# Kernel tuning notes

Hardware: AMD Instinct MI355X
Metric: run time of the kernel (lower is better)

Reference implementation:

```python
import jax, jax.numpy as jnp
import numpy as np

N_NODES = 50000
N_EDGES = 500000
IN_FEAT = 128
OUT_FEAT = 128
N_REL = 16


def setup_inputs() -> dict:
    key = jax.random.key(0)
    k1, k2, k3, k4 = jax.random.split(key, 4)
    entity_embeddings = jax.random.normal(k1, (N_NODES, IN_FEAT), dtype=jnp.float32)
    # xavier_uniform over (in, out) fan per relation slice
    limit = (6.0 / (IN_FEAT + OUT_FEAT)) ** 0.5
    weight = jax.random.uniform(k2, (N_REL, IN_FEAT, OUT_FEAT), dtype=jnp.float32,
                                minval=-limit, maxval=limit)
    edge_index = jax.random.randint(k3, (2, N_EDGES), 0, N_NODES, dtype=jnp.int64)
    edge_type = jax.random.randint(k4, (N_EDGES,), 0, N_REL, dtype=jnp.int64)
    return {"entity_embeddings": entity_embeddings, "weight": weight,
            "edge_index": edge_index, "edge_type": edge_type}


def reference(entity_embeddings, weight, edge_index, edge_type):
    # RGCN message passing: for each edge e with relation r:
    #   msg_e = x[src_e] @ W[r];  out[tgt_e] += msg_e;  out = relu(out)
    # Vectorized: transform every node by every relation once (R*N*in*out flops),
    # then gather the (relation, src) slice per edge and scatter-add to tgt.
    # This avoids gathering a per-edge (E, in, out) weight tensor.
    num_entities = entity_embeddings.shape[0]
    src = edge_index[0]
    tgt = edge_index[1]
    transformed = jnp.einsum('ni,rio->rno', entity_embeddings, weight)  # (R, N, O)
    msg = transformed[edge_type, src]                                   # (E, O)
    messages = jax.ops.segment_sum(msg, tgt, num_segments=num_entities)  # (N, O)
    # Dropout is identity in eval mode; reference omits it (deterministic baseline).
    return jax.nn.relu(messages)
```

## Files before the change

kernel.cpp:

```cpp
#include <hip/hip_runtime.h>
#include <hip/hip_bf16.h>

typedef __attribute__((ext_vector_type(8))) __bf16 bf16x8;
typedef __attribute__((ext_vector_type(4))) __bf16 bf16x4;
typedef __attribute__((ext_vector_type(4))) float f32x4;

#define IN_FEAT 128
#define OUT_FEAT 128
#define N_REL 16
#define TILE_M 64
#define CHUNK_T 4

__global__ __launch_bounds__(256) void prep_kernel(
        const float* __restrict__ w, __bf16* __restrict__ wt,
        const float* __restrict__ x, __bf16* __restrict__ xb, int nX, int cvtb,
        const int* __restrict__ etype, const int* __restrict__ etgt, int n,
        int* __restrict__ cnt_rel, int* __restrict__ cnt_tgt) {
    __shared__ __bf16 tile[32 * 136];
    __shared__ int h[N_REL];
    int t = threadIdx.x;
    if (blockIdx.x < 64) {
        int r = blockIdx.x >> 2;
        int n0 = (blockIdx.x & 3) * 32;
        const float* W = w + (size_t)r * IN_FEAT * OUT_FEAT;
        __bf16* T = wt + (size_t)r * IN_FEAT * OUT_FEAT;
        #pragma unroll
        for (int it = 0; it < 16; ++it) {
            int idx = t + it * 256;
            int k = idx >> 5, dn = idx & 31;
            tile[dn * 136 + k] = (__bf16)W[k * OUT_FEAT + n0 + dn];
        }
        __syncthreads();
        #pragma unroll
        for (int it = 0; it < 2; ++it) {
            int idx = t + it * 256;
            int nn = idx >> 4, c = idx & 15;
            bf16x8 v = *(const bf16x8*)(&tile[nn * 136 + c * 8]);
            *(bf16x8*)(T + (size_t)(n0 + nn) * IN_FEAT + c * 8) = v;
        }
    } else if (blockIdx.x < 64 + cvtb) {
        int i = ((blockIdx.x - 64) * 256 + t) * 8;
        if (i < nX) {
            const float4* xr = (const float4*)(x + i);
            float4 f0 = xr[0], f1 = xr[1];
            bf16x8 o = { (__bf16)f0.x, (__bf16)f0.y, (__bf16)f0.z, (__bf16)f0.w,
                         (__bf16)f1.x, (__bf16)f1.y, (__bf16)f1.z, (__bf16)f1.w };
            *(bf16x8*)(xb + i) = o;
        }
    } else {
        if (t < N_REL) h[t] = 0;
        __syncthreads();
        int stride = (gridDim.x - 64 - cvtb) * blockDim.x;
        for (int i = (blockIdx.x - 64 - cvtb) * blockDim.x + t; i < n; i += stride) {
            atomicAdd(&h[etype[i]], 1);
            atomicAdd(&cnt_tgt[etgt[i]], 1);
        }
        __syncthreads();
        if (t < N_REL) atomicAdd(&cnt_rel[t], h[t]);
    }
}

__global__ void hist_kernel(const int* __restrict__ etype, int n, int* __restrict__ cnt_rel) {
    __shared__ int h[N_REL];
    if (threadIdx.x < N_REL) h[threadIdx.x] = 0;
    __syncthreads();
    for (int i = blockIdx.x * blockDim.x + threadIdx.x; i < n; i += gridDim.x * blockDim.x)
        atomicAdd(&h[etype[i]], 1);
    __syncthreads();
    if (threadIdx.x < N_REL) atomicAdd(&cnt_rel[threadIdx.x], h[threadIdx.x]);
}
__global__ void prefix_kernel(const int* __restrict__ cnt, int* __restrict__ meta) {
    if (threadIdx.x == 0) {
        int off = 0, toff = 0;
        for (int r = 0; r < N_REL; ++r) {
            meta[r] = off; meta[32 + r] = toff; meta[64 + r] = off;
            off += cnt[r];
            toff += (cnt[r] + TILE_M - 1) / TILE_M;
        }
        meta[16] = off; meta[48] = toff;
    }
}

__global__ void scanA_kernel(const int* __restrict__ cnt, int n, int* __restrict__ partial) {
    __shared__ int s[256];
    int i = blockIdx.x * 256 + threadIdx.x;
    s[threadIdx.x] = (i < n) ? cnt[i] : 0;
    __syncthreads();
    for (int off = 128; off > 0; off >>= 1) {
        if (threadIdx.x < off) s[threadIdx.x] += s[threadIdx.x + off];
        __syncthreads();
    }
    if (threadIdx.x == 0) partial[blockIdx.x] = s[0];
}
__global__ void scanC2_kernel(const int* __restrict__ cnt, int n,
                              const int* __restrict__ partial,
                              const int* __restrict__ cnt_rel, int* __restrict__ meta,
                              int* __restrict__ base, int* __restrict__ cursor) {
    __shared__ int s[256];
    __shared__ int sbase;
    int t = threadIdx.x;
    int pb = 0;
    for (int i = t; i < (int)blockIdx.x; i += 256) pb += partial[i];
    s[t] = pb;
    __syncthreads();
    for (int off = 128; off > 0; off >>= 1) {
        if (t < off) s[t] += s[t + off];
        __syncthreads();
    }
    if (t == 0) sbase = s[0];
    __syncthreads();
    int blockbase = sbase;
    __syncthreads();
    int i = blockIdx.x * 256 + t;
    int v = (i < n) ? cnt[i] : 0;
    s[t] = v;
    __syncthreads();
    for (int off = 1; off < 256; off <<= 1) {
        int x = (t >= off) ? s[t - off] : 0;
        __syncthreads();
        s[t] += x;
        __syncthreads();
    }
    int b = blockbase + s[t] - v;
    if (i < n) { base[i] = b; cursor[i] = b; }
    if (blockIdx.x == 0 && t == 0) {
        int off = 0, toff = 0;
        for (int r = 0; r < N_REL; ++r) {
            meta[r] = off; meta[32 + r] = toff; meta[64 + r] = off;
            off += cnt_rel[r];
            toff += (cnt_rel[r] + TILE_M - 1) / TILE_M;
        }
        meta[16] = off; meta[48] = toff;
    }
}

#define SCATTER_EPT 2
#define SCATTER_CHUNK (256 * SCATTER_EPT)
__global__ __launch_bounds__(256) void scatter_slot_kernel(
        const int* __restrict__ esrc, const int* __restrict__ etgt,
        const int* __restrict__ etype, int n,
        int* __restrict__ cursor_rel, int* __restrict__ cursor_tgt,
        int* __restrict__ bsrc, int* __restrict__ bslot) {
    __shared__ int lcnt[N_REL];
    __shared__ int lbase[N_REL];
    int t = threadIdx.x;
    if (t < N_REL) lcnt[t] = 0;
    __syncthreads();
    int base = blockIdx.x * SCATTER_CHUNK;
    int rj[SCATTER_EPT], offj[SCATTER_EPT];
    #pragma unroll
    for (int j = 0; j < SCATTER_EPT; ++j) {
        int i = base + j * 256 + t;
        if (i < n) {
            int r = etype[i];
            rj[j] = r;
            offj[j] = atomicAdd(&lcnt[r], 1);
        } else rj[j] = -1;
    }
    __syncthreads();
    if (t < N_REL) lbase[t] = atomicAdd(&cursor_rel[t], lcnt[t]);
    __syncthreads();
    #pragma unroll
    for (int j = 0; j < SCATTER_EPT; ++j) {
        if (rj[j] >= 0) {
            int i = base + j * 256 + t;
            int p = lbase[rj[j]] + offj[j];
            bsrc[p] = esrc[i];
            bslot[p] = atomicAdd(&cursor_tgt[etgt[i]], 1);
        }
    }
}

__global__ __launch_bounds__(256) void scatter_kernel(
        const int* __restrict__ esrc, const int* __restrict__ etgt,
        const int* __restrict__ etype, int n,
        int* __restrict__ cursor,
        int* __restrict__ bsrc, int* __restrict__ btgt) {
    __shared__ int lcnt[N_REL];
    __shared__ int lbase[N_REL];
    int t = threadIdx.x;
    if (t < N_REL) lcnt[t] = 0;
    __syncthreads();
    int base = blockIdx.x * SCATTER_CHUNK;
    int rj[SCATTER_EPT], offj[SCATTER_EPT];
    #pragma unroll
    for (int j = 0; j < SCATTER_EPT; ++j) {
        int i = base + j * 256 + t;
        if (i < n) {
            int r = etype[i];
            rj[j] = r;
            offj[j] = atomicAdd(&lcnt[r], 1);
        } else rj[j] = -1;
    }
    __syncthreads();
    if (t < N_REL) lbase[t] = atomicAdd(&cursor[t], lcnt[t]);
    __syncthreads();
    #pragma unroll
    for (int j = 0; j < SCATTER_EPT; ++j) {
        if (rj[j] >= 0) {
            int i = base + j * 256 + t;
            int p = lbase[rj[j]] + offj[j];
            bsrc[p] = esrc[i];
            btgt[p] = etgt[i];
        }
    }
}

__global__ __launch_bounds__(256) void gemm_msg7_kernel(
    const __bf16* __restrict__ Xb,
    const __bf16* __restrict__ Wt,
    const int* __restrict__ bsrc, const int* __restrict__ bslot,
    const int* __restrict__ meta,
    __bf16* __restrict__ msg) {
    __shared__ __align__(16) __bf16 Bs[OUT_FEAT * 128];
    __shared__ __align__(16) __bf16 As[TILE_M * 128];
    __shared__ int s_slot[TILE_M];

    const int* rel_off = meta;
    const int* tile_pre = meta + 32;
    int T = tile_pre[16];
    int t0 = blockIdx.x * CHUNK_T;
    if (t0 >= T) return;
    int t1 = min(T, t0 + CHUNK_T);

    int tid = threadIdx.x;
    int wave = tid >> 6, lane = tid & 63;
    int q = lane >> 4, ln = lane & 15;
    uint4* BsV = (uint4*)Bs;
    uint4* AsV = (uint4*)As;
    const bf16x8* AsF = (const bf16x8*)As;
    const bf16x8* BsF = (const bf16x8*)Bs;

    int cur_rel = -1;
    for (int tt = t0; tt < t1; ++tt) {
        int rel = (cur_rel < 0) ? 0 : cur_rel;
        while (tt >= tile_pre[rel + 1]) ++rel;
        int tile = tt - tile_pre[rel];
        int row_start = rel_off[rel] + tile * TILE_M;
        int m_valid = min(TILE_M, rel_off[rel + 1] - row_start);

        __syncthreads();
        if (rel != cur_rel) {
            cur_rel = rel;
            const __bf16* wsrc = Wt + (size_t)rel * IN_FEAT * OUT_FEAT;
            #pragma unroll
            for (int i = 0; i < 8; ++i) {
                int cid = tid + i * 256;
                int row = cid >> 4, c = cid & 15;
                int feat = (row & 15) * 8 + (row >> 4);
                uint4 v = *(const uint4*)(wsrc + (size_t)feat * IN_FEAT + c * 8);
                BsV[row * 16 + (c ^ (row & 15))] = v;
            }
        }
        #pragma unroll
        for (int i = 0; i < 4; ++i) {
            int cid = tid + i * 256;
            int r = cid >> 4, c = cid & 15;
            int srcn = (r < m_valid) ? bsrc[row_start + r] : 0;
            uint4 v = *(const uint4*)(Xb + (size_t)srcn * IN_FEAT + c * 8);
            AsV[r * 16 + (c ^ (r & 15))] = v;
        }
        if (tid < TILE_M) s_slot[tid] = (tid < m_valid) ? bslot[row_start + tid] : -1;
        __syncthreads();

        f32x4 acc[8];
        f32x4 z = { 0.f, 0.f, 0.f, 0.f };
        #pragma unroll
        for (int nf = 0; nf < 8; ++nf) acc[nf] = z;

        int myrow = wave * 16 + ln;
        #pragma unroll
        for (int kk = 0; kk < 4; ++kk) {
            bf16x8 a = AsF[myrow * 16 + ((kk * 4 + q) ^ ln)];
            #pragma unroll
            for (int nf = 0; nf < 8; ++nf) {
                bf16x8 b = BsF[(nf * 16 + ln) * 16 + ((kk * 4 + q) ^ ln)];
                acc[nf] = __builtin_amdgcn_mfma_f32_16x16x32_bf16(a, b, acc[nf], 0, 0, 0);
            }
        }

        #pragma unroll
        for (int reg = 0; reg < 4; ++reg) {
            int row = wave * 16 + q * 4 + reg;
            int slot = s_slot[row];
            if (slot >= 0) {
                bf16x8 o = { (__bf16)acc[0][reg], (__bf16)acc[1][reg],
                             (__bf16)acc[2][reg], (__bf16)acc[3][reg],
                             (__bf16)acc[4][reg], (__bf16)acc[5][reg],
                             (__bf16)acc[6][reg], (__bf16)acc[7][reg] };
                *(bf16x8*)(msg + (size_t)slot * OUT_FEAT + ln * 8) = o;
            }
        }
    }
}

__global__ __launch_bounds__(256) void segsum4_kernel(
        const __bf16* __restrict__ msg, const int* __restrict__ base,
        int nnodes, int ntot, float* __restrict__ out) {
    int n = blockIdx.x * 4 + (threadIdx.x >> 6);
    if (n >= nnodes) return;
    int l = threadIdx.x & 63;
    int g = l >> 4, ln = l & 15;
    int s0 = base[n];
    int s1 = (n == nnodes - 1) ? ntot : base[n + 1];
    float a[8] = { 0.f, 0.f, 0.f, 0.f, 0.f, 0.f, 0.f, 0.f };
    for (int s = s0 + g; s < s1; s += 8) {
        bf16x8 m0 = *(const bf16x8*)(msg + (size_t)s * OUT_FEAT + ln * 8);
        if (s + 4 < s1) {
            bf16x8 m1 = *(const bf16x8*)(msg + (size_t)(s + 4) * OUT_FEAT + ln * 8);
            #pragma unroll
            for (int j = 0; j < 8; ++j) a[j] += (float)m0[j] + (float)m1[j];
        } else {
            #pragma unroll
            for (int j = 0; j < 8; ++j) a[j] += (float)m0[j];
        }
    }
    #pragma unroll
    for (int j = 0; j < 8; ++j) {
        a[j] += __shfl_xor(a[j], 16, 64);
        a[j] += __shfl_xor(a[j], 32, 64);
    }
    if (g == 0) {
        float4 o0 = { fmaxf(a[0], 0.f), fmaxf(a[1], 0.f), fmaxf(a[2], 0.f), fmaxf(a[3], 0.f) };
        float4 o1 = { fmaxf(a[4], 0.f), fmaxf(a[5], 0.f), fmaxf(a[6], 0.f), fmaxf(a[7], 0.f) };
        float* dst = out + (size_t)n * OUT_FEAT + ln * 8;
        *(float4*)dst = o0;
        *(float4*)(dst + 4) = o1;
    }
}

__global__ void cvtX_kernel(const float* __restrict__ x, __bf16* __restrict__ xb, int n) {
    int i = (blockIdx.x * blockDim.x + threadIdx.x) * 4;
    if (i < n) {
        float4 v = *(const float4*)(x + i);
        bf16x4 o = { (__bf16)v.x, (__bf16)v.y, (__bf16)v.z, (__bf16)v.w };
        *(bf16x4*)(xb + i) = o;
    }
}
#define LDA 136
__global__ __launch_bounds__(256) void gemm_scatter_kernel(
    const __bf16* __restrict__ Xb, const __bf16* __restrict__ Wt,
    const int* __restrict__ bsrc, const int* __restrict__ btgt,
    const int* __restrict__ meta, float* __restrict__ out) {
    __shared__ __align__(16) __bf16 As2[TILE_M * LDA];
    __shared__ __align__(16) __bf16 Bs2[OUT_FEAT * LDA];
    __shared__ int s_tgt[TILE_M];
    int bid = blockIdx.x;
    const int* rel_off = meta;
    const int* tile_pre = meta + 32;
    if (bid >= tile_pre[16]) return;
    int rel = 0;
    while (bid >= tile_pre[rel + 1]) rel++;
    int tile = bid - tile_pre[rel];
    int row_start = rel_off[rel] + tile * TILE_M;
    int m_valid = min(TILE_M, rel_off[rel + 1] - row_start);
    int t = threadIdx.x;
    {
        const __bf16* src = Wt + rel * IN_FEAT * OUT_FEAT;
        #pragma unroll
        for (int i = 0; i < 8; ++i) {
            int cid = t + i * 256;
            int n = cid >> 4, c = cid & 15;
            uint4 v = *(const uint4*)(src + n * IN_FEAT + c * 8);
            *(uint4*)(&Bs2[n * LDA + c * 8]) = v;
        }
    }
    {
        #pragma unroll
        for (int i = 0; i < 4; ++i) {
            int cid = t + i * 256;
            int r = cid >> 4, c = cid & 15;
            int srcn = (r < m_valid) ? bsrc[row_start + r] : 0;
            uint4 v = *(const uint4*)(Xb + srcn * IN_FEAT + c * 8);
            *(uint4*)(&As2[r * LDA + c * 8]) = v;
        }
        if (t < TILE_M) s_tgt[t] = (t < m_valid) ? btgt[row_start + t] : -1;
    }
    __syncthreads();
    int wave = t >> 6, lane = t & 63;
    int q = lane >> 4, ln = lane & 15;
    f32x4 acc[8];
    f32x4 z = { 0.f, 0.f, 0.f, 0.f };
    #pragma unroll
    for (int nf = 0; nf < 8; ++nf) acc[nf] = z;
    #pragma unroll
    for (int kk = 0; kk < 4; ++kk) {
        bf16x8 a = *(const bf16x8*)(&As2[(wave * 16 + ln) * LDA + kk * 32 + q * 8]);
        #pragma unroll
        for (int nf = 0; nf < 8; ++nf) {
            bf16x8 b = *(const bf16x8*)(&Bs2[(nf * 16 + ln) * LDA + kk * 32 + q * 8]);
            acc[nf] = __builtin_amdgcn_mfma_f32_16x16x32_bf16(a, b, acc[nf], 0, 0, 0);
        }
    }
    #pragma unroll
    for (int reg = 0; reg < 4; ++reg) {
        int r = wave * 16 + q * 4 + reg;
        int tgt = s_tgt[r];
        if (tgt >= 0) {
            float* orow = out + (size_t)tgt * OUT_FEAT + ln;
            #pragma unroll
            for (int nf = 0; nf < 8; ++nf)
                unsafeAtomicAdd(orow + nf * 16, acc[nf][reg]);
        }
    }
}
__global__ void relu_kernel(float* __restrict__ out, int n) {
    int i = (blockIdx.x * blockDim.x + threadIdx.x) * 4;
    if (i < n) {
        float4 v = *(float4*)(out + i);
        v.x = fmaxf(v.x, 0.f); v.y = fmaxf(v.y, 0.f);
        v.z = fmaxf(v.z, 0.f); v.w = fmaxf(v.w, 0.f);
        *(float4*)(out + i) = v;
    }
}

extern "C" void kernel_launch(void* const* d_in, const int* in_sizes, int n_in,
                              void* d_out, int out_size, void* d_ws, size_t ws_size,
                              hipStream_t stream) {
    const float* x = (const float*)d_in[0];
    const float* w = (const float*)d_in[1];
    const int* eidx = (const int*)d_in[2];
    const int* etype = (const int*)d_in[3];
    const int E = in_sizes[3];
    const int nX = in_sizes[0];
    const int N = out_size / OUT_FEAT;
    const int* esrc = eidx;
    const int* etgt = eidx + E;
    float* out = (float*)d_out;

    char* ws = (char*)d_ws;
    size_t off = 0;
    auto alloc = [&](size_t sz) { size_t o = off; off = (off + sz + 255) & ~(size_t)255; return o; };
    size_t off_Xb   = alloc((size_t)nX * 2);
    size_t off_Wt   = alloc((size_t)N_REL * IN_FEAT * OUT_FEAT * 2);
    size_t off_cnt  = alloc(64);
    size_t off_meta = alloc(512);
    size_t off_bsrc = alloc((size_t)E * 4);
    size_t off_bsl  = alloc((size_t)E * 4);
    size_t off_ctgt = alloc((size_t)(N + 16) * 4);
    size_t off_cur  = alloc((size_t)N * 4);
    size_t off_base = alloc((size_t)N * 4);
    size_t off_part = alloc(1024);
    size_t off_msg  = alloc((size_t)E * OUT_FEAT * 2);
    bool big = (ws_size >= off);

    __bf16* Xb = (__bf16*)(ws + off_Xb);
    __bf16* Wt = (__bf16*)(ws + off_Wt);
    int* meta  = (int*)(ws + off_meta);
    int* bsrc  = (int*)(ws + off_bsrc);
    int* bsl   = (int*)(ws + off_bsl);

    int scatter_blocks = (E + SCATTER_CHUNK - 1) / SCATTER_CHUNK;
    int max_tiles = (E + TILE_M - 1) / TILE_M + N_REL;

    if (big) {
        int* cnt_tgt = (int*)(ws + off_ctgt);
        int* cnt_rel = cnt_tgt + N;
        int* cursor  = (int*)(ws + off_cur);
        int* base    = (int*)(ws + off_base);
        int* partial = (int*)(ws + off_part);
        __bf16* msg  = (__bf16*)(ws + off_msg);
        int nchunks = (N + 255) / 256;
        int cvtb = (nX / 8 + 255) / 256;

        hipMemsetAsync(cnt_tgt, 0, (size_t)(N + 16) * 4, stream);
        prep_kernel<<<64 + cvtb + 1024, 256, 0, stream>>>(
            w, Wt, x, Xb, nX, cvtb, etype, etgt, E, cnt_rel, cnt_tgt);
        scanA_kernel<<<nchunks, 256, 0, stream>>>(cnt_tgt, N, partial);
        scanC2_kernel<<<nchunks, 256, 0, stream>>>(cnt_tgt, N, partial, cnt_rel, meta, base, cursor);
        scatter_slot_kernel<<<scatter_blocks, 256, 0, stream>>>(
            esrc, etgt, etype, E, meta + 64, cursor, bsrc, bsl);
        int gemm_blocks = (max_tiles + CHUNK_T - 1) / CHUNK_T;
        gemm_msg7_kernel<<<gemm_blocks, 256, 0, stream>>>(Xb, Wt, bsrc, bsl, meta, msg);
        segsum4_kernel<<<(N + 3) / 4, 256, 0, stream>>>(msg, base, N, E, out);
    } else {
        int* cnt = (int*)(ws + off_cnt);
        hipMemsetAsync(cnt, 0, 64, stream);
        hipMemsetAsync(out, 0, (size_t)out_size * 4, stream);
        cvtX_kernel<<<(nX / 4 + 255) / 256, 256, 0, stream>>>(x, Xb, nX);
        prep_kernel<<<64, 256, 0, stream>>>(w, Wt, x, Xb, 0, 0, etype, etgt, E, cnt, nullptr);
        hist_kernel<<<1024, 256, 0, stream>>>(etype, E, cnt);
        prefix_kernel<<<1, 64, 0, stream>>>(cnt, meta);
        scatter_kernel<<<scatter_blocks, 256, 0, stream>>>(
            esrc, etgt, etype, E, meta + 64, bsrc, bsl);
        gemm_scatter_kernel<<<max_tiles, 256, 0, stream>>>(Xb, Wt, bsrc, bsl, meta, out);
        relu_kernel<<<(out_size / 4 + 255) / 256, 256, 0, stream>>>(out, out_size);
    }
}
```

Baseline: 223.5 us.

## Fuse whole RGCN pipeline into one cooperative persistent kernel with grid syncs

Replaces the memset plus six separate kernel launches with a single cooperative kernel of 512 blocks. The stages (zeroing, weight transpose and X conversion, histogram, scan, scatter, GEMM, segment sum with ReLU) are separated by grid.sync() calls. The aim is to remove per-launch overhead and inter-kernel gaps. In exchange, each stage now runs on a fixed grid, so the GEMM and segsum stages use far fewer blocks than before, and the grid-wide barriers add their own cost. If the cooperative launch fails, the old multi-kernel path is used instead.

New measurement: 621.5 us. +178.1%, slower.

```diff
diff --git a/kernel.cpp b/kernel.cpp
--- a/kernel.cpp
+++ b/kernel.cpp
@@ -1,5 +1,8 @@
 #include <hip/hip_runtime.h>
 #include <hip/hip_bf16.h>
+#include <hip/hip_cooperative_groups.h>
+
+namespace cg = cooperative_groups;
 
 typedef __attribute__((ext_vector_type(8))) __bf16 bf16x8;
 typedef __attribute__((ext_vector_type(4))) __bf16 bf16x4;
@@ -9,7 +12,268 @@
 #define OUT_FEAT 128
 #define N_REL 16
 #define TILE_M 64
-#define CHUNK_T 4
+#define FUSED_GRID 512
+#define SCATTER_EPT 2
+#define SCATTER_CHUNK (256 * SCATTER_EPT)
+
+__global__ __launch_bounds__(256, 2) void fused_kernel(
+    const float* __restrict__ x, const float* __restrict__ w,
+    const int* __restrict__ esrc, const int* __restrict__ etgt,
+    const int* __restrict__ etype, int E, int N, int nX,
+    __bf16* __restrict__ Xb, __bf16* __restrict__ Wt,
+    int* __restrict__ cnt_tgt,
+    int* __restrict__ meta, int* __restrict__ bsrc, int* __restrict__ bslot,
+    int* __restrict__ base, int* __restrict__ cursor, int* __restrict__ partial,
+    __bf16* __restrict__ msg, float* __restrict__ out) {
+    cg::grid_group grid = cg::this_grid();
+    __shared__ __align__(16) char smem[49664];
+    int bid = blockIdx.x, t = threadIdx.x;
+    int* cnt_rel = cnt_tgt + N;
+
+    for (int i = bid * 256 + t; i < N + 16; i += FUSED_GRID * 256) cnt_tgt[i] = 0;
+    grid.sync();
+
+    if (bid < 64) {
+        __bf16* tile = (__bf16*)smem;
+        int r = bid >> 2, n0 = (bid & 3) * 32;
+        const float* W = w + (size_t)r * IN_FEAT * OUT_FEAT;
+        __bf16* Tw = Wt + (size_t)r * IN_FEAT * OUT_FEAT;
+        #pragma unroll
+        for (int it = 0; it < 16; ++it) {
+            int idx = t + it * 256;
+            int k = idx >> 5, dn = idx & 31;
+            tile[dn * 136 + k] = (__bf16)W[k * OUT_FEAT + n0 + dn];
+        }
+        __syncthreads();
+        #pragma unroll
+        for (int it = 0; it < 2; ++it) {
+            int idx = t + it * 256;
+            int nn = idx >> 4, c = idx & 15;
+            bf16x8 v = *(const bf16x8*)(&tile[nn * 136 + c * 8]);
+            *(bf16x8*)(Tw + (size_t)(n0 + nn) * IN_FEAT + c * 8) = v;
+        }
+    } else {
+        int U = nX >> 3;
+        for (int u = (bid - 64) * 256 + t; u < U; u += (FUSED_GRID - 64) * 256) {
+            const float4* xr = (const float4*)(x + (size_t)u * 8);
+            float4 f0 = xr[0], f1 = xr[1];
+            bf16x8 o = { (__bf16)f0.x, (__bf16)f0.y, (__bf16)f0.z, (__bf16)f0.w,
+                         (__bf16)f1.x, (__bf16)f1.y, (__bf16)f1.z, (__bf16)f1.w };
+            *(bf16x8*)(Xb + (size_t)u * 8) = o;
+        }
+    }
+    {
+        int* h = (int*)(smem + 9216);
+        __syncthreads();
+        if (t < N_REL) h[t] = 0;
+        __syncthreads();
+        for (int i = bid * 256 + t; i < E; i += FUSED_GRID * 256) {
+            atomicAdd(&h[etype[i]], 1);
+            atomicAdd(&cnt_tgt[etgt[i]], 1);
+        }
+        __syncthreads();
+        if (t < N_REL) atomicAdd(&cnt_rel[t], h[t]);
+    }
+    grid.sync();
+
+    int nchunks = (N + 255) >> 8;
+    if (bid < nchunks) {
+        int* s = (int*)smem;
+        int i = bid * 256 + t;
+        s[t] = (i < N) ? cnt_tgt[i] : 0;
+        __syncthreads();
+        for (int off = 128; off > 0; off >>= 1) {
+            if (t < off) s[t] += s[t + off];
+            __syncthreads();
+        }
+        if (t == 0) partial[bid] = s[0];
+    }
+    grid.sync();
+    if (bid == 0) {
+        int* s = (int*)smem;
+        int v = (t < nchunks) ? partial[t] : 0;
+        s[t] = v;
+        __syncthreads();
+        for (int off = 1; off < 256; off <<= 1) {
+            int xz = (t >= off) ? s[t - off] : 0;
+            __syncthreads();
+            s[t] += xz;
+            __syncthreads();
+        }
+        if (t < nchunks) partial[t] = s[t] - v;
+        if (t == 0) {
+            int off = 0, toff = 0;
+            for (int r = 0; r < N_REL; ++r) {
+                meta[r] = off; meta[32 + r] = toff; meta[64 + r] = off;
+                off += cnt_rel[r];
+                toff += (cnt_rel[r] + TILE_M - 1) / TILE_M;
+            }
+            meta[16] = off; meta[48] = toff;
+        }
+    }
+    grid.sync();
+    if (bid < nchunks) {
+        int* s = (int*)smem;
+        int i = bid * 256 + t;
+        int v = (i < N) ? cnt_tgt[i] : 0;
+        s[t] = v;
+        __syncthreads();
+        for (int off = 1; off < 256; off <<= 1) {
+            int xz = (t >= off) ? s[t - off] : 0;
+            __syncthreads();
+            s[t] += xz;
+            __syncthreads();
+        }
+        int b = partial[bid] + s[t] - v;
+        if (i < N) { base[i] = b; cursor[i] = b; }
+    }
+    grid.sync();
+    {
+        int* lcnt = (int*)smem;
+        int* lbase = (int*)(smem + 64);
+        int* cursor_rel = meta + 64;
+        int nsc = (E + SCATTER_CHUNK - 1) / SCATTER_CHUNK;
+        for (int c = bid; c < nsc; c += FUSED_GRID) {
+            __syncthreads();
+            if (t < N_REL) lcnt[t] = 0;
+            __syncthreads();
+            int cb = c * SCATTER_CHUNK;
+            int rj[SCATTER_EPT], offj[SCATTER_EPT];
+            #pragma unroll
+            for (int j = 0; j < SCATTER_EPT; ++j) {
+                int i = cb + j * 256 + t;
+                if (i < E) {
+                    int r = etype[i];
+                    rj[j] = r;
+                    offj[j] = atomicAdd(&lcnt[r], 1);
+                } else rj[j] = -1;
+            }
+            __syncthreads();
+            if (t < N_REL) lbase[t] = atomicAdd(&cursor_rel[t], lcnt[t]);
+            __syncthreads();
+            #pragma unroll
+            for (int j = 0; j < SCATTER_EPT; ++j) {
+                if (rj[j] >= 0) {
+                    int i = cb + j * 256 + t;
+                    int p = lbase[rj[j]] + offj[j];
+                    bsrc[p] = esrc[i];
+                    bslot[p] = atomicAdd(&cursor[etgt[i]], 1);
+                }
+            }
+        }
+    }
+    grid.sync();
+    {
+        const int* rel_off = meta;
+        const int* tile_pre = meta + 32;
+        int Tt = tile_pre[16];
+        int chunk = (Tt + FUSED_GRID - 1) / FUSED_GRID;
+        int t0 = bid * chunk, t1 = min(Tt, t0 + chunk);
+        __bf16* Bs = (__bf16*)smem;
+        __bf16* As = (__bf16*)(smem + 32768);
+        int* s_slot = (int*)(smem + 49152);
+        uint4* BsV = (uint4*)Bs;
+        uint4* AsV = (uint4*)As;
+        const bf16x8* AsF = (const bf16x8*)As;
+        const bf16x8* BsF = (const bf16x8*)Bs;
+        int wave = t >> 6, lane = t & 63;
+        int q = lane >> 4, ln = lane & 15;
+        int cur_rel = -1;
+        for (int tt = t0; tt < t1; ++tt) {
+            int rel = (cur_rel < 0) ? 0 : cur_rel;
+            while (tt >= tile_pre[rel + 1]) ++rel;
+            int row_start = rel_off[rel] + (tt - tile_pre[rel]) * TILE_M;
+            int m_valid = min(TILE_M, rel_off[rel + 1] - row_start);
+            __syncthreads();
+            if (rel != cur_rel) {
+                cur_rel = rel;
+                const __bf16* wsrc = Wt + (size_t)rel * IN_FEAT * OUT_FEAT;
+                #pragma unroll
+                for (int i = 0; i < 8; ++i) {
+                    int cid = t + i * 256;
+                    int row = cid >> 4, c = cid & 15;
+                    int feat = (row & 15) * 8 + (row >> 4);
+                    uint4 v = *(const uint4*)(wsrc + (size_t)feat * IN_FEAT + c * 8);
+                    BsV[row * 16 + (c ^ (row & 15))] = v;
+                }
+            }
+            #pragma unroll
+            for (int i = 0; i < 4; ++i) {
+                int cid = t + i * 256;
+                int r = cid >> 4, c = cid & 15;
+                int srcn = (r < m_valid) ? bsrc[row_start + r] : 0;
+                uint4 v = *(const uint4*)(Xb + (size_t)srcn * IN_FEAT + c * 8);
+                AsV[r * 16 + (c ^ (r & 15))] = v;
+            }
+            if (t < TILE_M) s_slot[t] = (t < m_valid) ? bslot[row_start + t] : -1;
+            __syncthreads();
+
+            f32x4 acc[8];
+            f32x4 z = { 0.f, 0.f, 0.f, 0.f };
+            #pragma unroll
+            for (int nf = 0; nf < 8; ++nf) acc[nf] = z;
+            int myrow = wave * 16 + ln;
+            #pragma unroll
+            for (int kk = 0; kk < 4; ++kk) {
+                bf16x8 a = AsF[myrow * 16 + ((kk * 4 + q) ^ ln)];
+                #pragma unroll
+                for (int nf = 0; nf < 8; ++nf) {
+                    bf16x8 b = BsF[(nf * 16 + ln) * 16 + ((kk * 4 + q) ^ ln)];
+                    acc[nf] = __builtin_amdgcn_mfma_f32_16x16x32_bf16(a, b, acc[nf], 0, 0, 0);
+                }
+            }
+            #pragma unroll
+            for (int reg = 0; reg < 4; ++reg) {
+                int row = wave * 16 + q * 4 + reg;
+                int slot = s_slot[row];
+                if (slot >= 0) {
+                    bf16x8 o = { (__bf16)acc[0][reg], (__bf16)acc[1][reg],
+                                 (__bf16)acc[2][reg], (__bf16)acc[3][reg],
+                                 (__bf16)acc[4][reg], (__bf16)acc[5][reg],
+                                 (__bf16)acc[6][reg], (__bf16)acc[7][reg] };
+                    *(bf16x8*)(msg + (size_t)slot * OUT_FEAT + ln * 8) = o;
+                }
+            }
+        }
+    }
+    grid.sync();
+    {
+        int ngrp = (N + 3) >> 2;
+        int wv = t >> 6, l = t & 63;
+        int g = l >> 4, ln = l & 15;
+        for (int grp = bid; grp < ngrp; grp += FUSED_GRID) {
+            int n = grp * 4 + wv;
+            if (n < N) {
+                int s0 = base[n];
+                int s1 = (n == N - 1) ? E : base[n + 1];
+                float a[8] = { 0.f, 0.f, 0.f, 0.f, 0.f, 0.f, 0.f, 0.f };
+                for (int s = s0 + g; s < s1; s += 8) {
+                    bf16x8 m0 = *(const bf16x8*)(msg + (size_t)s * OUT_FEAT + ln * 8);
+                    if (s + 4 < s1) {
+                        bf16x8 m1 = *(const bf16x8*)(msg + (size_t)(s + 4) * OUT_FEAT + ln * 8);
+                        #pragma unroll
+                        for (int j = 0; j < 8; ++j) a[j] += (float)m0[j] + (float)m1[j];
+                    } else {
+                        #pragma unroll
+                        for (int j = 0; j < 8; ++j) a[j] += (float)m0[j];
+                    }
+                }
+                #pragma unroll
+                for (int j = 0; j < 8; ++j) {
+                    a[j] += __shfl_xor(a[j], 16, 64);
+                    a[j] += __shfl_xor(a[j], 32, 64);
+                }
+                if (g == 0) {
+                    float4 o0 = { fmaxf(a[0], 0.f), fmaxf(a[1], 0.f), fmaxf(a[2], 0.f), fmaxf(a[3], 0.f) };
+                    float4 o1 = { fmaxf(a[4], 0.f), fmaxf(a[5], 0.f), fmaxf(a[6], 0.f), fmaxf(a[7], 0.f) };
+                    float* dst = out + (size_t)n * OUT_FEAT + ln * 8;
+                    *(float4*)dst = o0;
+                    *(float4*)(dst + 4) = o1;
+                }
+            }
+        }
+    }
+}
 
 __global__ __launch_bounds__(256) void prep_kernel(
         const float* __restrict__ w, __bf16* __restrict__ wt,
@@ -53,7 +317,7 @@
         int stride = (gridDim.x - 64 - cvtb) * blockDim.x;
         for (int i = (blockIdx.x - 64 - cvtb) * blockDim.x + t; i < n; i += stride) {
             atomicAdd(&h[etype[i]], 1);
-            atomicAdd(&cnt_tgt[etgt[i]], 1);
+            if (cnt_tgt) atomicAdd(&cnt_tgt[etgt[i]], 1);
         }
         __syncthreads();
         if (t < N_REL) atomicAdd(&cnt_rel[t], h[t]);
@@ -134,8 +398,6 @@
     }
 }
 
-#define SCATTER_EPT 2
-#define SCATTER_CHUNK (256 * SCATTER_EPT)
 __global__ __launch_bounds__(256) void scatter_slot_kernel(
         const int* __restrict__ esrc, const int* __restrict__ etgt,
         const int* __restrict__ etype, int n,
@@ -206,23 +468,20 @@
     }
 }
 
+#define CHUNK_T 4
 __global__ __launch_bounds__(256) void gemm_msg7_kernel(
-    const __bf16* __restrict__ Xb,
-    const __bf16* __restrict__ Wt,
+    const __bf16* __restrict__ Xb, const __bf16* __restrict__ Wt,
     const int* __restrict__ bsrc, const int* __restrict__ bslot,
-    const int* __restrict__ meta,
-    __bf16* __restrict__ msg) {
+    const int* __restrict__ meta, __bf16* __restrict__ msg) {
     __shared__ __align__(16) __bf16 Bs[OUT_FEAT * 128];
     __shared__ __align__(16) __bf16 As[TILE_M * 128];
     __shared__ int s_slot[TILE_M];
-
     const int* rel_off = meta;
     const int* tile_pre = meta + 32;
     int T = tile_pre[16];
     int t0 = blockIdx.x * CHUNK_T;
     if (t0 >= T) return;
     int t1 = min(T, t0 + CHUNK_T);
-
     int tid = threadIdx.x;
     int wave = tid >> 6, lane = tid & 63;
     int q = lane >> 4, ln = lane & 15;
@@ -230,15 +489,12 @@
     uint4* AsV = (uint4*)As;
     const bf16x8* AsF = (const bf16x8*)As;
     const bf16x8* BsF = (const bf16x8*)Bs;
-
     int cur_rel = -1;
     for (int tt = t0; tt < t1; ++tt) {
         int rel = (cur_rel < 0) ? 0 : cur_rel;
         while (tt >= tile_pre[rel + 1]) ++rel;
-        int tile = tt - tile_pre[rel];
-        int row_start = rel_off[rel] + tile * TILE_M;
+        int row_start = rel_off[rel] + (tt - tile_pre[rel]) * TILE_M;
         int m_valid = min(TILE_M, rel_off[rel + 1] - row_start);
-
         __syncthreads();
         if (rel != cur_rel) {
             cur_rel = rel;
@@ -262,12 +518,10 @@
         }
         if (tid < TILE_M) s_slot[tid] = (tid < m_valid) ? bslot[row_start + tid] : -1;
         __syncthreads();
-
         f32x4 acc[8];
         f32x4 z = { 0.f, 0.f, 0.f, 0.f };
         #pragma unroll
         for (int nf = 0; nf < 8; ++nf) acc[nf] = z;
-
         int myrow = wave * 16 + ln;
         #pragma unroll
         for (int kk = 0; kk < 4; ++kk) {
@@ -278,7 +532,6 @@
                 acc[nf] = __builtin_amdgcn_mfma_f32_16x16x32_bf16(a, b, acc[nf], 0, 0, 0);
             }
         }
-
         #pragma unroll
         for (int reg = 0; reg < 4; ++reg) {
             int row = wave * 16 + q * 4 + reg;
@@ -460,19 +713,30 @@
         int* base    = (int*)(ws + off_base);
         int* partial = (int*)(ws + off_part);
         __bf16* msg  = (__bf16*)(ws + off_msg);
-        int nchunks = (N + 255) / 256;
-        int cvtb = (nX / 8 + 255) / 256;
-
-        hipMemsetAsync(cnt_tgt, 0, (size_t)(N + 16) * 4, stream);
-        prep_kernel<<<64 + cvtb + 1024, 256, 0, stream>>>(
-            w, Wt, x, Xb, nX, cvtb, etype, etgt, E, cnt_rel, cnt_tgt);
-        scanA_kernel<<<nchunks, 256, 0, stream>>>(cnt_tgt, N, partial);
-        scanC2_kernel<<<nchunks, 256, 0, stream>>>(cnt_tgt, N, partial, cnt_rel, meta, base, cursor);
-        scatter_slot_kernel<<<scatter_blocks, 256, 0, stream>>>(
-            esrc, etgt, etype, E, meta + 64, cursor, bsrc, bsl);
-        int gemm_blocks = (max_tiles + CHUNK_T - 1) / CHUNK_T;
-        gemm_msg7_kernel<<<gemm_blocks, 256, 0, stream>>>(Xb, Wt, bsrc, bsl, meta, msg);
-        segsum4_kernel<<<(N + 3) / 4, 256, 0, stream>>>(msg, base, N, E, out);
+
+        int Ev = E, Nv = N, nXv = nX;
+        void* args[] = { (void*)&x, (void*)&w, (void*)&esrc, (void*)&etgt, (void*)&etype,
+                         (void*)&Ev, (void*)&Nv, (void*)&nXv,
+                         (void*)&Xb, (void*)&Wt, (void*)&cnt_tgt, (void*)&meta,
+                         (void*)&bsrc, (void*)&bsl, (void*)&base, (void*)&cursor,
+                         (void*)&partial, (void*)&msg, (void*)&out };
+        hipError_t cerr = hipLaunchCooperativeKernel(
+            (const void*)fused_kernel, dim3(FUSED_GRID), dim3(256), args, 0, stream);
+        if (cerr != hipSuccess) {
+            (void)hipGetLastError();
+            int nchunks = (N + 255) / 256;
+            int cvtb = (nX / 8 + 255) / 256;
+            hipMemsetAsync(cnt_tgt, 0, (size_t)(N + 16) * 4, stream);
+            prep_kernel<<<64 + cvtb + 1024, 256, 0, stream>>>(
+                w, Wt, x, Xb, nX, cvtb, etype, etgt, E, cnt_rel, cnt_tgt);
+            scanA_kernel<<<nchunks, 256, 0, stream>>>(cnt_tgt, N, partial);
+            scanC2_kernel<<<nchunks, 256, 0, stream>>>(cnt_tgt, N, partial, cnt_rel, meta, base, cursor);
+            scatter_slot_kernel<<<scatter_blocks, 256, 0, stream>>>(
+                esrc, etgt, etype, E, meta + 64, cursor, bsrc, bsl);
+            int gemm_blocks = (max_tiles + CHUNK_T - 1) / CHUNK_T;
+            gemm_msg7_kernel<<<gemm_blocks, 256, 0, stream>>>(Xb, Wt, bsrc, bsl, meta, msg);
+            segsum4_kernel<<<(N + 3) / 4, 256, 0, stream>>>(msg, base, N, E, out);
+        }
     } else {
         int* cnt = (int*)(ws + off_cnt);
         hipMemsetAsync(cnt, 0, 64, stream);
```

## Load gathered A fragments directly into registers, drop A tile from LDS

Applied to the files above, without the earlier changes.

The gather GEMM kernel no longer stages the gathered source rows in shared memory. Each lane loads its MFMA A fragments straight from global memory and keeps the slot indices in registers. This removes two per-tile barriers and the A/slot shared buffers, shrinking LDS use so more blocks can be resident, and the launch bounds now request 4 blocks per SM. Each block also handles 8 tiles instead of 4, so the relation weights are reloaded less often, at the cost of fewer blocks and uncoalesced per-lane row loads. A null check on the target-count histogram is added as well.

After: 208.6 us. -6.6%, faster.

```diff
diff --git a/kernel.cpp b/kernel.cpp
--- a/kernel.cpp
+++ b/kernel.cpp
@@ -9,7 +9,7 @@
 #define OUT_FEAT 128
 #define N_REL 16
 #define TILE_M 64
-#define CHUNK_T 4
+#define CHUNK_T 8
 
 __global__ __launch_bounds__(256) void prep_kernel(
         const float* __restrict__ w, __bf16* __restrict__ wt,
@@ -53,7 +53,7 @@
         int stride = (gridDim.x - 64 - cvtb) * blockDim.x;
         for (int i = (blockIdx.x - 64 - cvtb) * blockDim.x + t; i < n; i += stride) {
             atomicAdd(&h[etype[i]], 1);
-            atomicAdd(&cnt_tgt[etgt[i]], 1);
+            if (cnt_tgt) atomicAdd(&cnt_tgt[etgt[i]], 1);
         }
         __syncthreads();
         if (t < N_REL) atomicAdd(&cnt_rel[t], h[t]);
@@ -206,16 +206,13 @@
     }
 }
 
-__global__ __launch_bounds__(256) void gemm_msg7_kernel(
+__global__ __launch_bounds__(256, 4) void gemm_msg8_kernel(
     const __bf16* __restrict__ Xb,
     const __bf16* __restrict__ Wt,
     const int* __restrict__ bsrc, const int* __restrict__ bslot,
     const int* __restrict__ meta,
     __bf16* __restrict__ msg) {
     __shared__ __align__(16) __bf16 Bs[OUT_FEAT * 128];
-    __shared__ __align__(16) __bf16 As[TILE_M * 128];
-    __shared__ int s_slot[TILE_M];
-
     const int* rel_off = meta;
     const int* tile_pre = meta + 32;
     int T = tile_pre[16];
@@ -227,20 +224,18 @@
     int wave = tid >> 6, lane = tid & 63;
     int q = lane >> 4, ln = lane & 15;
     uint4* BsV = (uint4*)Bs;
-    uint4* AsV = (uint4*)As;
-    const bf16x8* AsF = (const bf16x8*)As;
     const bf16x8* BsF = (const bf16x8*)Bs;
+    int myrow = wave * 16 + ln;
 
     int cur_rel = -1;
     for (int tt = t0; tt < t1; ++tt) {
         int rel = (cur_rel < 0) ? 0 : cur_rel;
         while (tt >= tile_pre[rel + 1]) ++rel;
-        int tile = tt - tile_pre[rel];
-        int row_start = rel_off[rel] + tile * TILE_M;
+        int row_start = rel_off[rel] + (tt - tile_pre[rel]) * TILE_M;
         int m_valid = min(TILE_M, rel_off[rel + 1] - row_start);
 
-        __syncthreads();
         if (rel != cur_rel) {
+            if (cur_rel >= 0) __syncthreads();
             cur_rel = rel;
             const __bf16* wsrc = Wt + (size_t)rel * IN_FEAT * OUT_FEAT;
             #pragma unroll
@@ -251,44 +246,45 @@
                 uint4 v = *(const uint4*)(wsrc + (size_t)feat * IN_FEAT + c * 8);
                 BsV[row * 16 + (c ^ (row & 15))] = v;
             }
-        }
-        #pragma unroll
-        for (int i = 0; i < 4; ++i) {
-            int cid = tid + i * 256;
-            int r = cid >> 4, c = cid & 15;
-            int srcn = (r < m_valid) ? bsrc[row_start + r] : 0;
-            uint4 v = *(const uint4*)(Xb + (size_t)srcn * IN_FEAT + c * 8);
-            AsV[r * 16 + (c ^ (r & 15))] = v;
-        }
-        if (tid < TILE_M) s_slot[tid] = (tid < m_valid) ? bslot[row_start + tid] : -1;
-        __syncthreads();
+            __syncthreads();
+        }
+
+        int src = bsrc[row_start + min(myrow, m_valid - 1)];
+        const __bf16* xrow = Xb + (size_t)src * IN_FEAT;
+        bf16x8 afr[4];
+        #pragma unroll
+        for (int kk = 0; kk < 4; ++kk)
+            afr[kk] = *(const bf16x8*)(xrow + (kk * 4 + q) * 8);
+
+        int slot[4];
+        #pragma unroll
+        for (int reg = 0; reg < 4; ++reg) {
+            int r = wave * 16 + q * 4 + reg;
+            slot[reg] = (r < m_valid) ? bslot[row_start + r] : -1;
+        }
 
         f32x4 acc[8];
         f32x4 z = { 0.f, 0.f, 0.f, 0.f };
         #pragma unroll
         for (int nf = 0; nf < 8; ++nf) acc[nf] = z;
 
-        int myrow = wave * 16 + ln;
         #pragma unroll
         for (int kk = 0; kk < 4; ++kk) {
-            bf16x8 a = AsF[myrow * 16 + ((kk * 4 + q) ^ ln)];
             #pragma unroll
             for (int nf = 0; nf < 8; ++nf) {
                 bf16x8 b = BsF[(nf * 16 + ln) * 16 + ((kk * 4 + q) ^ ln)];
-                acc[nf] = __builtin_amdgcn_mfma_f32_16x16x32_bf16(a, b, acc[nf], 0, 0, 0);
+                acc[nf] = __builtin_amdgcn_mfma_f32_16x16x32_bf16(afr[kk], b, acc[nf], 0, 0, 0);
             }
         }
 
         #pragma unroll
         for (int reg = 0; reg < 4; ++reg) {
-            int row = wave * 16 + q * 4 + reg;
-            int slot = s_slot[row];
-            if (slot >= 0) {
+            if (slot[reg] >= 0) {
                 bf16x8 o = { (__bf16)acc[0][reg], (__bf16)acc[1][reg],
                              (__bf16)acc[2][reg], (__bf16)acc[3][reg],
                              (__bf16)acc[4][reg], (__bf16)acc[5][reg],
                              (__bf16)acc[6][reg], (__bf16)acc[7][reg] };
-                *(bf16x8*)(msg + (size_t)slot * OUT_FEAT + ln * 8) = o;
+                *(bf16x8*)(msg + (size_t)slot[reg] * OUT_FEAT + ln * 8) = o;
             }
         }
     }
@@ -471,7 +467,7 @@
         scatter_slot_kernel<<<scatter_blocks, 256, 0, stream>>>(
             esrc, etgt, etype, E, meta + 64, cursor, bsrc, bsl);
         int gemm_blocks = (max_tiles + CHUNK_T - 1) / CHUNK_T;
-        gemm_msg7_kernel<<<gemm_blocks, 256, 0, stream>>>(Xb, Wt, bsrc, bsl, meta, msg);
+        gemm_msg8_kernel<<<gemm_blocks, 256, 0, stream>>>(Xb, Wt, bsrc, bsl, meta, msg);
         segsum4_kernel<<<(N + 3) / 4, 256, 0, stream>>>(msg, base, N, E, out);
     } else {
         int* cnt = (int*)(ws + off_cnt);
```
